# Kernel optimization log

Hardware: AMD Instinct MI355X
Metric: run time of the kernel (lower is better)

## Reference

```python
import jax, jax.numpy as jnp
import numpy as np

T, D, H, C = 8, 512, 100, 2  # n_edge_types, dim_in_time+dim_in_node, hidden(=100 in source), predict_class
E, NEG = 100000, 1


def _linear_params(key, fan_in, fan_out, n_types):
    k1, k2 = jax.random.split(key)
    bound = 1.0 / np.sqrt(fan_in)
    W = jax.random.uniform(k1, (n_types, fan_in, fan_out), jnp.float32, -bound, bound)
    b = jax.random.uniform(k2, (n_types, fan_out), jnp.float32, -bound, bound)
    return W, b


def setup_inputs() -> dict:
    key = jax.random.key(0)
    kh, kt, k1, k2, k3 = jax.random.split(key, 5)
    h = jax.random.normal(kh, ((NEG + 2) * E, D), jnp.float32)
    edge_types = jax.random.randint(kt, (E,), 0, T).astype(jnp.int32)
    src_W, src_b = _linear_params(k1, D, H, T)
    dst_W, dst_b = _linear_params(k2, D, H, T)
    out_W, out_b = _linear_params(k3, H, C, T)
    return {"h": h, "src_W": src_W, "src_b": src_b, "dst_W": dst_W,
            "dst_b": dst_b, "out_W": out_W, "out_b": out_b,
            "edge_types": edge_types, "neg_samples": NEG}


def _select_type(all_types, t):
    # all_types: [N, T, F], t: [N] int -> [N, F]
    return jnp.take_along_axis(all_types, t[:, None, None], axis=1)[:, 0]


def reference(h, src_W, src_b, dst_W, dst_b, out_W, out_b, edge_types, neg_samples):
    num_edge = edge_types.shape[0]
    h_src = h[:num_edge]                      # [E, D]
    h_pos_dst = h[num_edge:2 * num_edge]      # [E, D]
    h_neg_dst = h[2 * num_edge:]              # [E*neg, D]
    h_save = h[:2 * num_edge]
    t = edge_types
    t_neg = jnp.repeat(t, neg_samples)        # type of each neg row

    # type-routed linears: compute for all types, then select per-edge type
    src_enc = _select_type(jnp.einsum('ed,tdh->eth', h_src, src_W) + src_b[None], t)          # [E, H]
    pos_enc = _select_type(jnp.einsum('ed,tdh->eth', h_pos_dst, dst_W) + dst_b[None], t)      # [E, H]
    neg_enc = _select_type(jnp.einsum('ed,tdh->eth', h_neg_dst, dst_W) + dst_b[None], t_neg)  # [E*neg, H]

    pos_edge = jax.nn.relu(src_enc + pos_enc)
    neg_edge = jax.nn.relu(jnp.repeat(src_enc, neg_samples, axis=0) + neg_enc)

    pos_out = _select_type(jnp.einsum('eh,thc->etc', pos_edge, out_W) + out_b[None], t)       # [E, C]
    neg_out = _select_type(jnp.einsum('eh,thc->etc', neg_edge, out_W) + out_b[None], t_neg)   # [E*neg, C]

    # source concatenates per-type groups in type order (stable within a type)
    perm = jnp.argsort(t, stable=True)
    pos_pred = pos_out[perm]
    neg_idx = (perm[:, None] * neg_samples + jnp.arange(neg_samples)).reshape(-1)
    neg_pred = neg_out[neg_idx]
    return pos_pred, neg_pred, h_save
```

## Files before the change

kernel.cpp:

```cpp
#include <hip/hip_runtime.h>

constexpr int D_ = 512;
constexpr int H_ = 100;
constexpr int C_ = 2;
constexpr int T_ = 8;

constexpr int TE  = 128;
constexpr int DC  = 32;
constexpr int NC  = D_ / DC;
constexpr int NTH = 256;
constexpr int GRID_MAIN = 256;
constexpr int SB  = 128;
constexpr int STH = 256;

constexpr int WS_CTR  = 26;
constexpr int WS_HIST = 32;
constexpr int WS_SORTED = 32 + SB * T_;
constexpr int WS_WPRE = 131072;

typedef __attribute__((ext_vector_type(8))) short bf16x8;
typedef __attribute__((ext_vector_type(4))) float f32x4;

__device__ __forceinline__ unsigned short bfhi(float x) {
    return (unsigned short)(__builtin_bit_cast(unsigned int, x) >> 16);
}
__device__ __forceinline__ float bfback(unsigned short u) {
    return __builtin_bit_cast(float, (unsigned int)u << 16);
}

__global__ __launch_bounds__(STH) void k_hist(const int* __restrict__ et, int E, int seg,
                                              int* __restrict__ hist) {
    __shared__ int hb[T_];
    const int b = blockIdx.x, tid = threadIdx.x;
    if (tid < T_) hb[tid] = 0;
    __syncthreads();
    const int segLo = b * seg;
    const int segHi = min(E, segLo + seg);
    const int per = (seg + STH - 1) / STH;
    const int lo = segLo + tid * per;
    const int hi = min(segHi, lo + per);
    int c[T_];
#pragma unroll
    for (int j = 0; j < T_; ++j) c[j] = 0;
    for (int i = lo; i < hi; ++i) {
        int ty = et[i];
#pragma unroll
        for (int j = 0; j < T_; ++j) c[j] += (ty == j) ? 1 : 0;
    }
#pragma unroll
    for (int j = 0; j < T_; ++j)
        if (c[j]) atomicAdd(&hb[j], c[j]);
    __syncthreads();
    if (tid < T_) hist[b * T_ + tid] = hb[tid];
}

__global__ __launch_bounds__(SB) void k_scan(int* __restrict__ hist,
                                             int* __restrict__ typeBase,
                                             int* __restrict__ typeCount,
                                             int* __restrict__ tileBase,
                                             int* __restrict__ ctr, int grid0) {
    __shared__ int sc[SB][T_ + 1];
    __shared__ int sbase[T_];
    const int tid = threadIdx.x;
#pragma unroll
    for (int j = 0; j < T_; ++j) sc[tid][j] = hist[tid * T_ + j];
    __syncthreads();
    for (int ofs = 1; ofs < SB; ofs <<= 1) {
        int v[T_];
        if (tid >= ofs) {
#pragma unroll
            for (int j = 0; j < T_; ++j) v[j] = sc[tid - ofs][j];
        }
        __syncthreads();
        if (tid >= ofs) {
#pragma unroll
            for (int j = 0; j < T_; ++j) sc[tid][j] += v[j];
        }
        __syncthreads();
    }
    if (tid == 0) {
        int b = 0, tb = 0;
#pragma unroll
        for (int j = 0; j < T_; ++j) {
            int cntj = sc[SB - 1][j];
            sbase[j] = b;
            typeBase[j] = b;
            typeCount[j] = cntj;
            tileBase[j] = tb;
            b += cntj;
            tb += (cntj + TE - 1) / TE;
        }
        tileBase[T_] = tb;
        ctr[0] = grid0;
    }
    __syncthreads();
#pragma unroll
    for (int j = 0; j < T_; ++j)
        hist[tid * T_ + j] = sbase[j] + (tid ? sc[tid - 1][j] : 0);
}

__global__ __launch_bounds__(STH) void k_scatter(const int* __restrict__ et, int E, int seg,
                                                 const int* __restrict__ blockBase,
                                                 int* __restrict__ sorted_e) {
    __shared__ int sc[STH][T_ + 1];
    const int b = blockIdx.x, tid = threadIdx.x;
    const int segLo = b * seg;
    const int segHi = min(E, segLo + seg);
    const int per = (seg + STH - 1) / STH;
    const int lo = segLo + tid * per;
    const int hi = min(segHi, lo + per);
    int c[T_];
#pragma unroll
    for (int j = 0; j < T_; ++j) c[j] = 0;
    for (int i = lo; i < hi; ++i) {
        int ty = et[i];
#pragma unroll
        for (int j = 0; j < T_; ++j) c[j] += (ty == j) ? 1 : 0;
    }
#pragma unroll
    for (int j = 0; j < T_; ++j) sc[tid][j] = c[j];
    __syncthreads();
    for (int ofs = 1; ofs < STH; ofs <<= 1) {
        int v[T_];
        if (tid >= ofs) {
#pragma unroll
            for (int j = 0; j < T_; ++j) v[j] = sc[tid - ofs][j];
        }
        __syncthreads();
        if (tid >= ofs) {
#pragma unroll
            for (int j = 0; j < T_; ++j) sc[tid][j] += v[j];
        }
        __syncthreads();
    }
    int p[T_];
#pragma unroll
    for (int j = 0; j < T_; ++j)
        p[j] = blockBase[b * T_ + j] + (tid ? sc[tid - 1][j] : 0);
    for (int i = lo; i < hi; ++i) {
        int ty = et[i];
        int r = 0;
#pragma unroll
        for (int j = 0; j < T_; ++j) {
            if (ty == j) { r = p[j]; p[j] = r + 1; }
        }
        sorted_e[r] = i;
    }
}

__global__ __launch_bounds__(256) void k_prew(const float* __restrict__ srcW,
                                              const float* __restrict__ dstW,
                                              unsigned* __restrict__ wPre) {
    const int flat = blockIdx.x * 256 + threadIdx.x;
    const int n    = flat % 112;
    int rest = flat / 112;
    const int lgm = rest % 8;
    const int mat = lgm >> 2, lg = lgm & 3;
    rest /= 8;
    const int ch = rest % 16, t = rest / 16;

    float x[8];
    if (n < H_) {
        const float* W = (mat ? dstW : srcW) + (size_t)t * D_ * H_
                       + (size_t)(ch * 32 + lg * 8) * H_ + n;
#pragma unroll
        for (int j = 0; j < 8; ++j) x[j] = W[(size_t)j * H_];
    } else {
#pragma unroll
        for (int j = 0; j < 8; ++j) x[j] = 0.f;
    }
    unsigned hu[4], lu[4];
#pragma unroll
    for (int p = 0; p < 4; ++p) {
        float x0 = x[2 * p], x1 = x[2 * p + 1];
        unsigned short h0 = bfhi(x0), h1 = bfhi(x1);
        unsigned short l0 = bfhi(x0 - bfback(h0));
        unsigned short l1 = bfhi(x1 - bfback(h1));
        hu[p] = (unsigned)h0 | ((unsigned)h1 << 16);
        lu[p] = (unsigned)l0 | ((unsigned)l1 << 16);
    }
    const int slot = n ^ ((n >> 3) & 7);
    const unsigned bse = (unsigned)(t * 16 + ch) * 7168u;
    unsigned hiA = bse + (unsigned)(((mat * 2 + 0) * 4 + lg) * 448 + slot * 4);
    unsigned loA = bse + (unsigned)(((mat * 2 + 1) * 4 + lg) * 448 + slot * 4);
    *(uint4*)&wPre[hiA] = (uint4){hu[0], hu[1], hu[2], hu[3]};
    *(uint4*)&wPre[loA] = (uint4){lu[0], lu[1], lu[2], lu[3]};
}

__device__ __forceinline__ float fold16(float (&v)[16], int ln) {
    float v8[8];
#pragma unroll
    for (int a = 0; a < 8; ++a) {
        float keep = (ln & 1) ? v[2 * a + 1] : v[2 * a];
        float send = (ln & 1) ? v[2 * a] : v[2 * a + 1];
        v8[a] = keep + __shfl_xor(send, 1);
    }
    float v4[4];
#pragma unroll
    for (int a = 0; a < 4; ++a) {
        float keep = (ln & 2) ? v8[2 * a + 1] : v8[2 * a];
        float send = (ln & 2) ? v8[2 * a] : v8[2 * a + 1];
        v4[a] = keep + __shfl_xor(send, 2);
    }
    float v2[2];
#pragma unroll
    for (int a = 0; a < 2; ++a) {
        float keep = (ln & 4) ? v4[2 * a + 1] : v4[2 * a];
        float send = (ln & 4) ? v4[2 * a] : v4[2 * a + 1];
        v2[a] = keep + __shfl_xor(send, 4);
    }
    float keep = (ln & 8) ? v2[1] : v2[0];
    float send = (ln & 8) ? v2[0] : v2[1];
    return keep + __shfl_xor(send, 8);
}

__global__ __launch_bounds__(NTH, 1) void k_main(
    const float* __restrict__ h,
    const float* __restrict__ srcB, const float* __restrict__ dstB,
    const float* __restrict__ outW, const float* __restrict__ outB,
    const int* __restrict__ sorted_e,
    const int* __restrict__ typeBase, const int* __restrict__ typeCount,
    const int* __restrict__ tileBase,
    const unsigned* __restrict__ wPre,
    int* __restrict__ ctr,
    float* __restrict__ out, int E)
{
    const int tid = threadIdx.x;
    const int w   = tid >> 6;
    const int l   = tid & 63;
    const int ln  = l & 15;
    const int lg  = l >> 4;

    __shared__ __align__(16) float4 stgH[2][3 * TE * (DC / 4)];
    __shared__ __align__(16) unsigned wB[2][7168];
    __shared__ int eIdx[TE];
    __shared__ int sNext;

    const int nT = tileBase[T_];
    const size_t mStride = (size_t)E * D_;
    float* const outH = out + (size_t)4 * E;

    int tile = blockIdx.x;
    while (tile < nT) {
        int t = 0;
#pragma unroll
        for (int j = 1; j < T_; ++j) t += (tile >= tileBase[j]) ? 1 : 0;
        const int i0   = (tile - tileBase[t]) * TE;
        const int cnt  = typeCount[t];
        const int base = typeBase[t];

        if (tid < TE) {
            int p = i0 + tid;
            eIdx[tid] = sorted_e[base + (p < cnt ? p : i0)];
        }
        __syncthreads();

        const int r0 = tid >> 3, s8 = tid & 7;
        const float* rowSrc[4]; float* rowHS[4]; int slotLin[4]; bool gok[4];
#pragma unroll
        for (int rr4 = 0; rr4 < 4; ++rr4) {
            int rr = r0 + rr4 * 32;
            int sw = (rr ^ (rr >> 3)) & 7;
            int c4 = s8 ^ sw;
            int e  = eIdx[rr];
            rowSrc[rr4]  = h    + (size_t)e * D_ + (c4 << 2);
            rowHS[rr4]   = outH + (size_t)e * D_ + (s8 << 2);
            slotLin[rr4] = rr * 8 + c4;
            gok[rr4]     = (i0 + rr) < cnt;
        }

        const float4* const wPreT = (const float4*)(wPre + (size_t)t * 16 * 7168);

        auto stageH = [&](int buf, int d0c) {
            float4* dH = &stgH[buf][0];
#pragma unroll
            for (int m = 0; m < 3; ++m)
#pragma unroll
                for (int rr4 = 0; rr4 < 4; ++rr4)
                    __builtin_amdgcn_global_load_lds(
                        (const __attribute__((address_space(1))) void*)(rowSrc[rr4] + m * mStride + d0c),
                        (__attribute__((address_space(3))) void*)(dH + m * 1024 + rr4 * 256 + tid),
                        16, 0, 0);
        };
        auto stageW = [&](int buf, int chl) {
            const float4* src = wPreT + chl * 1792;
            float4* dst = (float4*)&wB[buf][0];
#pragma unroll
            for (int it = 0; it < 7; ++it)
                __builtin_amdgcn_global_load_lds(
                    (const __attribute__((address_space(1))) void*)(src + it * 256 + tid),
                    (__attribute__((address_space(3))) void*)(dst + it * 256 + tid),
                    16, 0, 0);
        };

        f32x4 acc[6][7];
#pragma unroll
        for (int a = 0; a < 6; ++a)
#pragma unroll
            for (int nt = 0; nt < 7; ++nt) acc[a][nt] = (f32x4){0.f, 0.f, 0.f, 0.f};

        stageH(0, 0);
        stageW(0, 0);

#pragma unroll 1
        for (int ch = 0; ch < NC; ++ch) {
            const int d0 = ch * DC;
            const int cb = ch & 1;

            __syncthreads();

            if (ch + 1 < NC) {
                stageH(cb ^ 1, d0 + DC);
                stageW(cb ^ 1, ch + 1);
            }

            const float4* csH = &stgH[cb][0];

#pragma unroll
            for (int m = 0; m < 2; ++m)
#pragma unroll
                for (int rr4 = 0; rr4 < 4; ++rr4) {
                    float4 v = csH[m * 1024 + slotLin[rr4]];
                    if (gok[rr4]) *(float4*)(rowHS[rr4] + m * mStride + d0) = v;
                }

            bf16x8 Ahi[6], Alo[6];
#pragma unroll
            for (int a = 0; a < 6; ++a) {
                const int row = (w + 4 * a) * 16 + ln;
                const int swR = (row ^ (row >> 3)) & 7;
                const float4* rp = csH + row * 8;
                float4 x0 = rp[(2 * lg) ^ swR];
                float4 x1 = rp[(2 * lg + 1) ^ swR];
#pragma unroll
                for (int j = 0; j < 4; ++j) {
                    float v0 = ((const float*)&x0)[j];
                    unsigned short hh = bfhi(v0);
                    Ahi[a][j] = (short)hh;
                    Alo[a][j] = (short)bfhi(v0 - bfback(hh));
                }
#pragma unroll
                for (int j = 0; j < 4; ++j) {
                    float v1 = ((const float*)&x1)[j];
                    unsigned short hh = bfhi(v1);
                    Ahi[a][4 + j] = (short)hh;
                    Alo[a][4 + j] = (short)bfhi(v1 - bfback(hh));
                }
            }

#pragma unroll
            for (int nt = 0; nt < 7; ++nt) {
                const int n = nt * 16 + ln;
                const int slotP = n ^ ((n >> 3) & 7);
                bf16x8 B[2][2];
#pragma unroll
                for (int mat = 0; mat < 2; ++mat)
#pragma unroll
                    for (int hl = 0; hl < 2; ++hl)
                        B[mat][hl] = *(const bf16x8*)&wB[cb][(((mat * 2 + hl) * 4 + lg) * 112 + slotP) * 4];
#pragma unroll
                for (int a = 0; a < 6; ++a) {
                    const int mm = (a < 2) ? 0 : 1;
                    acc[a][nt] = __builtin_amdgcn_mfma_f32_16x16x32_bf16(Ahi[a], B[mm][0], acc[a][nt], 0, 0, 0);
                    acc[a][nt] = __builtin_amdgcn_mfma_f32_16x16x32_bf16(Ahi[a], B[mm][1], acc[a][nt], 0, 0, 0);
                    acc[a][nt] = __builtin_amdgcn_mfma_f32_16x16x32_bf16(Alo[a], B[mm][0], acc[a][nt], 0, 0, 0);
                }
            }
        }

        float sB7[7], dB7[7], woA[7], woB[7];
        bool valn[7];
#pragma unroll
        for (int nt = 0; nt < 7; ++nt) {
            int n = nt * 16 + ln;
            valn[nt] = (n < H_);
            int nc = valn[nt] ? n : (H_ - 1);
            sB7[nt] = srcB[t * H_ + nc];
            dB7[nt] = dstB[t * H_ + nc];
            float2 wo = *(const float2*)(outW + (size_t)t * H_ * C_ + nc * C_);
            woA[nt] = wo.x; woB[nt] = wo.y;
        }

        float pp[16], nn[16];
#pragma unroll
        for (int i = 0; i < 16; ++i) { pp[i] = 0.f; nn[i] = 0.f; }
#pragma unroll
        for (int nt = 0; nt < 7; ++nt)
#pragma unroll
            for (int a = 0; a < 2; ++a)
#pragma unroll
                for (int reg = 0; reg < 4; ++reg) {
                    float sv = acc[a][nt][reg] + sB7[nt] + dB7[nt];
                    float pe = fmaxf(acc[a + 2][nt][reg] + sv, 0.f);
                    float ne = fmaxf(acc[a + 4][nt][reg] + sv, 0.f);
                    pe = valn[nt] ? pe : 0.f;
                    ne = valn[nt] ? ne : 0.f;
                    const int ix = a * 8 + reg * 2;
                    pp[ix]     = fmaf(pe, woA[nt], pp[ix]);
                    pp[ix + 1] = fmaf(pe, woB[nt], pp[ix + 1]);
                    nn[ix]     = fmaf(ne, woA[nt], nn[ix]);
                    nn[ix + 1] = fmaf(ne, woB[nt], nn[ix + 1]);
                }

        float totP = fold16(pp, ln);
        float totN = fold16(nn, ln);
        {
            const int c   = ln & 1;
            const int reg = (ln >> 1) & 3;
            const int aa  = (ln >> 3) & 1;
            const int e   = (w + 4 * aa) * 16 + lg * 4 + reg;
            if (i0 + e < cnt) {
                float ob = outB[t * C_ + c];
                size_t pidx = (size_t)(base + i0 + e) * C_ + c;
                out[pidx] = totP + ob;
                out[(size_t)C_ * E + pidx] = totN + ob;
            }
        }

        __syncthreads();
        if (tid == 0) sNext = atomicAdd(ctr, 1);
        __syncthreads();
        tile = sNext;
    }
}

extern "C" void kernel_launch(void* const* d_in, const int* in_sizes, int n_in,
                              void* d_out, int out_size, void* d_ws, size_t ws_size,
                              hipStream_t stream) {
    (void)n_in; (void)out_size; (void)ws_size;
    const float* h    = (const float*)d_in[0];
    const float* srcW = (const float*)d_in[1];
    const float* srcB = (const float*)d_in[2];
    const float* dstW = (const float*)d_in[3];
    const float* dstB = (const float*)d_in[4];
    const float* outW = (const float*)d_in[5];
    const float* outB = (const float*)d_in[6];
    const int*   et   = (const int*)d_in[7];
    const int E = in_sizes[7];

    float* out = (float*)d_out;
    int* ws = (int*)d_ws;
    int* typeBase  = ws;
    int* typeCount = ws + 8;
    int* tileBase  = ws + 16;
    int* ctr       = ws + WS_CTR;
    int* hist      = ws + WS_HIST;
    int* sorted_e  = ws + WS_SORTED;
    unsigned* wPre = (unsigned*)(ws + WS_WPRE);

    const int seg = (E + SB - 1) / SB;
    k_hist<<<SB, STH, 0, stream>>>(et, E, seg, hist);
    k_scan<<<1, SB, 0, stream>>>(hist, typeBase, typeCount, tileBase, ctr, GRID_MAIN);
    k_scatter<<<SB, STH, 0, stream>>>(et, E, seg, hist, sorted_e);
    k_prew<<<448, 256, 0, stream>>>(srcW, dstW, wPre);

    k_main<<<GRID_MAIN, NTH, 0, stream>>>(h, srcB, dstB, outW, outB,
                                          sorted_e, typeBase, typeCount, tileBase,
                                          wPre, ctr, out, E);
}
```

Baseline: 1.049 ms.

## Halve edge tile, widen K chunk, and hand-schedule split weight staging

The edge tile shrinks from 128 to 64 rows and the D chunk grows from 32 to 64. The MFMA accumulator array halves, which frees registers for higher occupancy. Weight slices are now staged per 32-wide half-chunk into alternating LDS buffers, and `__syncthreads` is replaced by explicit `s_waitcnt vmcnt`/barrier sequences so loads overlap the two k-steps more finely. In exchange, per-edge weight traffic roughly doubles, there are twice as many tiles to schedule, and the h_save copy no longer checks whether each row is past the end of its type group.

```diff
diff --git a/kernel.cpp b/kernel.cpp
--- a/kernel.cpp
+++ b/kernel.cpp
@@ -5,8 +5,8 @@
 constexpr int C_ = 2;
 constexpr int T_ = 8;
 
-constexpr int TE  = 128;
-constexpr int DC  = 32;
+constexpr int TE  = 64;
+constexpr int DC  = 64;
 constexpr int NC  = D_ / DC;
 constexpr int NTH = 256;
 constexpr int GRID_MAIN = 256;
@@ -27,6 +27,12 @@
 __device__ __forceinline__ float bfback(unsigned short u) {
     return __builtin_bit_cast(float, (unsigned int)u << 16);
 }
+__device__ __forceinline__ int swz16(int r) { return (r ^ (r >> 3)) & 15; }
+
+#define KBAR(NSTR) do { \
+    asm volatile("s_waitcnt vmcnt(" NSTR ") lgkmcnt(0)\n\ts_barrier" ::: "memory"); \
+    __builtin_amdgcn_sched_barrier(0); \
+} while (0)
 
 __global__ __launch_bounds__(STH) void k_hist(const int* __restrict__ et, int E, int seg,
                                               int* __restrict__ hist) {
@@ -157,12 +163,12 @@
     const int lgm = rest % 8;
     const int mat = lgm >> 2, lg = lgm & 3;
     rest /= 8;
-    const int ch = rest % 16, t = rest / 16;
+    const int s = rest % 16, t = rest / 16;
 
     float x[8];
     if (n < H_) {
         const float* W = (mat ? dstW : srcW) + (size_t)t * D_ * H_
-                       + (size_t)(ch * 32 + lg * 8) * H_ + n;
+                       + (size_t)(s * 32 + lg * 8) * H_ + n;
 #pragma unroll
         for (int j = 0; j < 8; ++j) x[j] = W[(size_t)j * H_];
     } else {
@@ -180,7 +186,7 @@
         lu[p] = (unsigned)l0 | ((unsigned)l1 << 16);
     }
     const int slot = n ^ ((n >> 3) & 7);
-    const unsigned bse = (unsigned)(t * 16 + ch) * 7168u;
+    const unsigned bse = (unsigned)(t * 16 + s) * 7168u;
     unsigned hiA = bse + (unsigned)(((mat * 2 + 0) * 4 + lg) * 448 + slot * 4);
     unsigned loA = bse + (unsigned)(((mat * 2 + 1) * 4 + lg) * 448 + slot * 4);
     *(uint4*)&wPre[hiA] = (uint4){hu[0], hu[1], hu[2], hu[3]};
@@ -240,6 +246,10 @@
     const size_t mStride = (size_t)E * D_;
     float* const outH = out + (size_t)4 * E;
 
+    const int rA = w * 16 + ln;
+    const int Sa = swz16(rA);
+    const int aBase = rA * 16;
+
     int tile = blockIdx.x;
     while (tile < nT) {
         int t = 0;
@@ -255,18 +265,20 @@
         }
         __syncthreads();
 
-        const int r0 = tid >> 3, s8 = tid & 7;
-        const float* rowSrc[4]; float* rowHS[4]; int slotLin[4]; bool gok[4];
-#pragma unroll
-        for (int rr4 = 0; rr4 < 4; ++rr4) {
-            int rr = r0 + rr4 * 32;
-            int sw = (rr ^ (rr >> 3)) & 7;
-            int c4 = s8 ^ sw;
-            int e  = eIdx[rr];
-            rowSrc[rr4]  = h    + (size_t)e * D_ + (c4 << 2);
-            rowHS[rr4]   = outH + (size_t)e * D_ + (s8 << 2);
-            slotLin[rr4] = rr * 8 + c4;
-            gok[rr4]     = (i0 + rr) < cnt;
+        const int rT  = tid >> 4;
+        const int s16 = tid & 15;
+        const float* rowS4[4];
+        float*       rowH4[4];
+        int          slotL4[4];
+#pragma unroll
+        for (int rg = 0; rg < 4; ++rg) {
+            int r  = rg * 16 + rT;
+            int S  = swz16(r);
+            int c16 = s16 ^ S;
+            int e  = eIdx[r];
+            rowS4[rg]  = h    + (size_t)e * D_ + (c16 << 2);
+            rowH4[rg]  = outH + (size_t)e * D_ + (s16 << 2);
+            slotL4[rg] = r * 16 + c16;
         }
 
         const float4* const wPreT = (const float4*)(wPre + (size_t)t * 16 * 7168);
@@ -276,14 +288,14 @@
 #pragma unroll
             for (int m = 0; m < 3; ++m)
 #pragma unroll
-                for (int rr4 = 0; rr4 < 4; ++rr4)
+                for (int rg = 0; rg < 4; ++rg)
                     __builtin_amdgcn_global_load_lds(
-                        (const __attribute__((address_space(1))) void*)(rowSrc[rr4] + m * mStride + d0c),
-                        (__attribute__((address_space(3))) void*)(dH + m * 1024 + rr4 * 256 + tid),
+                        (const __attribute__((address_space(1))) void*)(rowS4[rg] + m * mStride + d0c),
+                        (__attribute__((address_space(3))) void*)(dH + m * 1024 + rg * 256 + tid),
                         16, 0, 0);
         };
-        auto stageW = [&](int buf, int chl) {
-            const float4* src = wPreT + chl * 1792;
+        auto stageW = [&](int buf, int s) {
+            const float4* src = wPreT + s * 1792;
             float4* dst = (float4*)&wB[buf][0];
 #pragma unroll
             for (int it = 0; it < 7; ++it)
@@ -293,127 +305,125 @@
                     16, 0, 0);
         };
 
-        f32x4 acc[6][7];
-#pragma unroll
-        for (int a = 0; a < 6; ++a)
-#pragma unroll
-            for (int nt = 0; nt < 7; ++nt) acc[a][nt] = (f32x4){0.f, 0.f, 0.f, 0.f};
+        f32x4 acc[3][7];
+#pragma unroll
+        for (int m = 0; m < 3; ++m)
+#pragma unroll
+            for (int nt = 0; nt < 7; ++nt) acc[m][nt] = (f32x4){0.f, 0.f, 0.f, 0.f};
+
+        auto kstep = [&](const float4* cs, int j) {
+            bf16x8 Ahi[3], Alo[3];
+#pragma unroll
+            for (int m = 0; m < 3; ++m) {
+                const float4* rp = cs + m * 1024 + aBase;
+                float4 x0 = rp[(j * 8 + 2 * lg) ^ Sa];
+                float4 x1 = rp[(j * 8 + 2 * lg + 1) ^ Sa];
+#pragma unroll
+                for (int q = 0; q < 4; ++q) {
+                    float v0 = ((const float*)&x0)[q];
+                    unsigned short hh = bfhi(v0);
+                    Ahi[m][q] = (short)hh;
+                    Alo[m][q] = (short)bfhi(v0 - bfback(hh));
+                }
+#pragma unroll
+                for (int q = 0; q < 4; ++q) {
+                    float v1 = ((const float*)&x1)[q];
+                    unsigned short hh = bfhi(v1);
+                    Ahi[m][4 + q] = (short)hh;
+                    Alo[m][4 + q] = (short)bfhi(v1 - bfback(hh));
+                }
+            }
+#pragma unroll
+            for (int nt = 0; nt < 7; ++nt) {
+                const int n = nt * 16 + ln;
+                const int slotP = n ^ ((n >> 3) & 7);
+                bf16x8 B[2][2];
+#pragma unroll
+                for (int mat = 0; mat < 2; ++mat)
+#pragma unroll
+                    for (int hl = 0; hl < 2; ++hl)
+                        B[mat][hl] = *(const bf16x8*)&wB[j][(((mat * 2 + hl) * 4 + lg) * 112 + slotP) * 4];
+#pragma unroll
+                for (int m = 0; m < 3; ++m) {
+                    const int mm = (m == 0) ? 0 : 1;
+                    acc[m][nt] = __builtin_amdgcn_mfma_f32_16x16x32_bf16(Ahi[m], B[mm][0], acc[m][nt], 0, 0, 0);
+                    acc[m][nt] = __builtin_amdgcn_mfma_f32_16x16x32_bf16(Ahi[m], B[mm][1], acc[m][nt], 0, 0, 0);
+                    acc[m][nt] = __builtin_amdgcn_mfma_f32_16x16x32_bf16(Alo[m], B[mm][0], acc[m][nt], 0, 0, 0);
+                }
+            }
+        };
 
         stageH(0, 0);
         stageW(0, 0);
+        KBAR("0");
 
 #pragma unroll 1
         for (int ch = 0; ch < NC; ++ch) {
             const int d0 = ch * DC;
             const int cb = ch & 1;
-
-            __syncthreads();
-
-            if (ch + 1 < NC) {
-                stageH(cb ^ 1, d0 + DC);
-                stageW(cb ^ 1, ch + 1);
+            const float4* cs = &stgH[cb][0];
+
+            stageW(1, 2 * ch + 1);
+            if (ch + 1 < NC) stageH(cb ^ 1, d0 + DC);
+#pragma unroll
+            for (int m = 0; m < 2; ++m)
+#pragma unroll
+                for (int rg = 0; rg < 4; ++rg) {
+                    float4 v = cs[m * 1024 + slotL4[rg]];
+                    *(float4*)(rowH4[rg] + m * mStride + d0) = v;
+                }
+            kstep(cs, 0);
+
+            if (ch < NC - 1) KBAR("20");
+            else             KBAR("8");
+
+            if (ch + 1 < NC) stageW(0, 2 * ch + 2);
+            kstep(cs, 1);
+
+            KBAR("0");
+        }
+
+        {
+            float sB7[7], dB7[7], woA[7], woB[7];
+            bool valn[7];
+#pragma unroll
+            for (int nt = 0; nt < 7; ++nt) {
+                int n = nt * 16 + ln;
+                valn[nt] = (n < H_);
+                int nc = valn[nt] ? n : (H_ - 1);
+                sB7[nt] = srcB[t * H_ + nc];
+                dB7[nt] = dstB[t * H_ + nc];
+                float2 wo = *(const float2*)(outW + (size_t)t * H_ * C_ + nc * C_);
+                woA[nt] = wo.x; woB[nt] = wo.y;
             }
 
-            const float4* csH = &stgH[cb][0];
-
-#pragma unroll
-            for (int m = 0; m < 2; ++m)
-#pragma unroll
-                for (int rr4 = 0; rr4 < 4; ++rr4) {
-                    float4 v = csH[m * 1024 + slotLin[rr4]];
-                    if (gok[rr4]) *(float4*)(rowHS[rr4] + m * mStride + d0) = v;
-                }
-
-            bf16x8 Ahi[6], Alo[6];
-#pragma unroll
-            for (int a = 0; a < 6; ++a) {
-                const int row = (w + 4 * a) * 16 + ln;
-                const int swR = (row ^ (row >> 3)) & 7;
-                const float4* rp = csH + row * 8;
-                float4 x0 = rp[(2 * lg) ^ swR];
-                float4 x1 = rp[(2 * lg + 1) ^ swR];
-#pragma unroll
-                for (int j = 0; j < 4; ++j) {
-                    float v0 = ((const float*)&x0)[j];
-                    unsigned short hh = bfhi(v0);
-                    Ahi[a][j] = (short)hh;
-                    Alo[a][j] = (short)bfhi(v0 - bfback(hh));
-                }
-#pragma unroll
-                for (int j = 0; j < 4; ++j) {
-                    float v1 = ((const float*)&x1)[j];
-                    unsigned short hh = bfhi(v1);
-                    Ahi[a][4 + j] = (short)hh;
-                    Alo[a][4 + j] = (short)bfhi(v1 - bfback(hh));
-                }
-            }
-
-#pragma unroll
-            for (int nt = 0; nt < 7; ++nt) {
-                const int n = nt * 16 + ln;
-                const int slotP = n ^ ((n >> 3) & 7);
-                bf16x8 B[2][2];
-#pragma unroll
-                for (int mat = 0; mat < 2; ++mat)
-#pragma unroll
-                    for (int hl = 0; hl < 2; ++hl)
-                        B[mat][hl] = *(const bf16x8*)&wB[cb][(((mat * 2 + hl) * 4 + lg) * 112 + slotP) * 4];
-#pragma unroll
-                for (int a = 0; a < 6; ++a) {
-                    const int mm = (a < 2) ? 0 : 1;
-                    acc[a][nt] = __builtin_amdgcn_mfma_f32_16x16x32_bf16(Ahi[a], B[mm][0], acc[a][nt], 0, 0, 0);
-                    acc[a][nt] = __builtin_amdgcn_mfma_f32_16x16x32_bf16(Ahi[a], B[mm][1], acc[a][nt], 0, 0, 0);
-                    acc[a][nt] = __builtin_amdgcn_mfma_f32_16x16x32_bf16(Alo[a], B[mm][0], acc[a][nt], 0, 0, 0);
-                }
-            }
-        }
-
-        float sB7[7], dB7[7], woA[7], woB[7];
-        bool valn[7];
-#pragma unroll
-        for (int nt = 0; nt < 7; ++nt) {
-            int n = nt * 16 + ln;
-            valn[nt] = (n < H_);
-            int nc = valn[nt] ? n : (H_ - 1);
-            sB7[nt] = srcB[t * H_ + nc];
-            dB7[nt] = dstB[t * H_ + nc];
-            float2 wo = *(const float2*)(outW + (size_t)t * H_ * C_ + nc * C_);
-            woA[nt] = wo.x; woB[nt] = wo.y;
-        }
-
-        float pp[16], nn[16];
-#pragma unroll
-        for (int i = 0; i < 16; ++i) { pp[i] = 0.f; nn[i] = 0.f; }
-#pragma unroll
-        for (int nt = 0; nt < 7; ++nt)
-#pragma unroll
-            for (int a = 0; a < 2; ++a)
+            float v16[16];
+#pragma unroll
+            for (int i = 0; i < 16; ++i) v16[i] = 0.f;
+#pragma unroll
+            for (int nt = 0; nt < 7; ++nt)
 #pragma unroll
                 for (int reg = 0; reg < 4; ++reg) {
-                    float sv = acc[a][nt][reg] + sB7[nt] + dB7[nt];
-                    float pe = fmaxf(acc[a + 2][nt][reg] + sv, 0.f);
-                    float ne = fmaxf(acc[a + 4][nt][reg] + sv, 0.f);
+                    float sv = acc[0][nt][reg] + sB7[nt] + dB7[nt];
+                    float pe = fmaxf(acc[1][nt][reg] + sv, 0.f);
+                    float ne = fmaxf(acc[2][nt][reg] + sv, 0.f);
                     pe = valn[nt] ? pe : 0.f;
                     ne = valn[nt] ? ne : 0.f;
-                    const int ix = a * 8 + reg * 2;
-                    pp[ix]     = fmaf(pe, woA[nt], pp[ix]);
-                    pp[ix + 1] = fmaf(pe, woB[nt], pp[ix + 1]);
-                    nn[ix]     = fmaf(ne, woA[nt], nn[ix]);
-                    nn[ix + 1] = fmaf(ne, woB[nt], nn[ix + 1]);
+                    v16[reg * 2 + 0]     = fmaf(pe, woA[nt], v16[reg * 2 + 0]);
+                    v16[reg * 2 + 1]     = fmaf(pe, woB[nt], v16[reg * 2 + 1]);
+                    v16[8 + reg * 2 + 0] = fmaf(ne, woA[nt], v16[8 + reg * 2 + 0]);
+                    v16[8 + reg * 2 + 1] = fmaf(ne, woB[nt], v16[8 + reg * 2 + 1]);
                 }
 
-        float totP = fold16(pp, ln);
-        float totN = fold16(nn, ln);
-        {
+            float tot = fold16(v16, ln);
             const int c   = ln & 1;
             const int reg = (ln >> 1) & 3;
-            const int aa  = (ln >> 3) & 1;
-            const int e   = (w + 4 * aa) * 16 + lg * 4 + reg;
+            const int pn  = ln >> 3;
+            const int e   = w * 16 + lg * 4 + reg;
             if (i0 + e < cnt) {
-                float ob = outB[t * C_ + c];
+                float val = tot + outB[t * C_ + c];
                 size_t pidx = (size_t)(base + i0 + e) * C_ + c;
-                out[pidx] = totP + ob;
-                out[(size_t)C_ * E + pidx] = totN + ob;
+                out[(pn ? (size_t)C_ * E : (size_t)0) + pidx] = val;
             }
         }
 
```

Measured after the change: 1.036 ms. About the same (-1.3%).
